# Performance work log

Hardware: AMD Instinct MI355X
Metric: run time of the kernel (lower is better)

## Reference

```python
import jax, jax.numpy as jnp
import numpy as np

B, S, D = 4, 2048, 1024
E, H, TOP_K = 8, 4096, 2


def setup_inputs() -> dict:
    key = jax.random.key(0)
    ks = jax.random.split(key, 5)
    scale = 0.02
    return {
        "x": jax.random.normal(ks[0], (B, S, D), dtype=jnp.float32),
        "Wr": jax.random.normal(ks[1], (D, E), dtype=jnp.float32) * scale,
        "br": jnp.zeros((E,), dtype=jnp.float32),
        "W1": jax.random.normal(ks[2], (E, D, H), dtype=jnp.float32) * scale,
        "b1": jnp.zeros((E, H), dtype=jnp.float32),
        "W2": jax.random.normal(ks[3], (E, H, D), dtype=jnp.float32) * scale,
        "b2": jnp.zeros((E, D), dtype=jnp.float32),
    }


def reference(x, Wr, br, W1, b1, W2, b2):
    b, s, d = x.shape
    xf = x.reshape(-1, d)                                   # [T, D]
    gate = jax.nn.softmax(xf @ Wr + br, axis=-1)            # [T, E]
    top_w, top_i = jax.lax.top_k(gate, TOP_K)               # [T, K]
    top_w = top_w / jnp.sum(top_w, axis=-1, keepdims=True)
    # combine[t, e] = sum_i top_w[t, i] * 1{top_i[t, i] == e}
    combine = jnp.sum(jax.nn.one_hot(top_i, E, dtype=xf.dtype) * top_w[..., None], axis=1)  # [T, E]
    # Dense all-expert FFN (same math as the masked per-expert loops in torch)
    h = jax.nn.gelu(jnp.einsum('td,edh->teh', xf, W1) + b1, approximate=False)  # [T, E, H]
    out = jnp.einsum('teh,ehd,te->td', h, W2, combine) + combine @ b2           # [T, D]
    return out.reshape(b, s, d)
```

## Files before the change

kernel.cpp:

```cpp
#include <hip/hip_runtime.h>
#include <cstdio>


#define T_TOK 8192
#define DIM   1024
#define NEXP  8
#define HID   4096
#define MAXR  18432

typedef float          f32x4   __attribute__((ext_vector_type(4)));
typedef short          bf16x8  __attribute__((ext_vector_type(8)));
typedef unsigned short u16x8   __attribute__((ext_vector_type(8)));
typedef unsigned short u16x4   __attribute__((ext_vector_type(4)));

static __device__ __forceinline__ unsigned short f2bf(float f) {
  unsigned int u = __builtin_bit_cast(unsigned int, f);
  u = (u + 0x7FFFu + ((u >> 16) & 1u)) >> 16;
  return (unsigned short)u;
}

static __device__ __forceinline__ void gl16(const void* g, void* l) {
  __builtin_amdgcn_global_load_lds(
      (const __attribute__((address_space(1))) unsigned int*)g,
      (__attribute__((address_space(3))) unsigned int*)l,
      16, 0, 0);
}

static __device__ __forceinline__ void transpose_body(const float* __restrict__ W,
                                                      unsigned short* __restrict__ WT,
                                                      int R, int C, int bx, int by, int e,
                                                      unsigned int* tl) {
  int t = threadIdx.x;
  int r0 = by * 128, c0 = bx * 128;
  const float* src = W + (size_t)e * R * C + (size_t)r0 * C + c0;
  int cg = t & 31, ph = t >> 5;
  int c4 = cg * 4;
#pragma unroll
  for (int u = 0; u < 8; ++u) {
    int p = u * 8 + ph;
    float4 f0 = *(const float4*)(src + (size_t)(2 * p) * C + c4);
    float4 f1 = *(const float4*)(src + (size_t)(2 * p + 1) * C + c4);
    unsigned int v0 = ((unsigned)f2bf(f1.x) << 16) | f2bf(f0.x);
    unsigned int v1 = ((unsigned)f2bf(f1.y) << 16) | f2bf(f0.y);
    unsigned int v2 = ((unsigned)f2bf(f1.z) << 16) | f2bf(f0.z);
    unsigned int v3 = ((unsigned)f2bf(f1.w) << 16) | f2bf(f0.w);
    *(uint4*)(tl + p * 132 + c4) = make_uint4(v0, v1, v2, v3);
  }
  __syncthreads();
  int rg = t & 15, ch = t >> 4;
  unsigned short* dst = WT + (size_t)e * R * C + (size_t)c0 * R + r0 + rg * 8;
#pragma unroll
  for (int u = 0; u < 8; ++u) {
    int c = ch + u * 16;
    u16x8 o;
#pragma unroll
    for (int j = 0; j < 4; ++j) {
      unsigned int v = tl[(rg * 4 + j) * 132 + c];
      o[2 * j]     = (unsigned short)(v & 0xffff);
      o[2 * j + 1] = (unsigned short)(v >> 16);
    }
    *(u16x8*)(dst + (size_t)c * R) = o;
  }
}

static __device__ __forceinline__ void router_body(int blk, const float* __restrict__ x,
                                                   const float* __restrict__ Wr,
                                                   const float* __restrict__ br,
                                                   int* __restrict__ meta,
                                                   int2* __restrict__ top_i,
                                                   float2* __restrict__ top_w) {
  int lane = threadIdx.x & 63;
  int wid  = threadIdx.x >> 6;
  int t = blk * 4 + wid;
  const float* xp = x + (size_t)t * DIM + lane * 16;
  float acc[NEXP];
#pragma unroll
  for (int e = 0; e < NEXP; ++e) acc[e] = 0.f;
#pragma unroll
  for (int j = 0; j < 16; j += 4) {
    float4 xv = *(const float4*)(xp + j);
    const float* wp = Wr + (size_t)(lane * 16 + j) * NEXP;
#pragma unroll
    for (int jj = 0; jj < 4; ++jj) {
      float xs = jj == 0 ? xv.x : jj == 1 ? xv.y : jj == 2 ? xv.z : xv.w;
      float4 w0 = *(const float4*)(wp + jj * NEXP);
      float4 w1 = *(const float4*)(wp + jj * NEXP + 4);
      acc[0] += xs * w0.x; acc[1] += xs * w0.y; acc[2] += xs * w0.z; acc[3] += xs * w0.w;
      acc[4] += xs * w1.x; acc[5] += xs * w1.y; acc[6] += xs * w1.z; acc[7] += xs * w1.w;
    }
  }
#pragma unroll
  for (int off = 32; off > 0; off >>= 1) {
#pragma unroll
    for (int e = 0; e < NEXP; ++e) acc[e] += __shfl_xor(acc[e], off);
  }
  if (lane == 0) {
    float l[NEXP];
#pragma unroll
    for (int e = 0; e < NEXP; ++e) l[e] = acc[e] + br[e];
    int e1 = 0;
#pragma unroll
    for (int e = 1; e < NEXP; ++e) if (l[e] > l[e1]) e1 = e;
    int e2 = (e1 == 0) ? 1 : 0;
#pragma unroll
    for (int e = 0; e < NEXP; ++e) if (e != e1 && l[e] > l[e2]) e2 = e;
    float g  = expf(l[e2] - l[e1]);
    float w1 = 1.f / (1.f + g);
    top_i[t] = make_int2(e1, e2);
    top_w[t] = make_float2(w1, 1.f - w1);
    atomicAdd(&meta[e1], 1);
    atomicAdd(&meta[e2], 1);
  }
}

__global__ __launch_bounds__(256) void prep_k(const float* __restrict__ W1,
                                              const float* __restrict__ W2,
                                              unsigned short* __restrict__ W1bT,
                                              unsigned short* __restrict__ W2bT,
                                              const float* __restrict__ x,
                                              const float* __restrict__ Wr,
                                              const float* __restrict__ br,
                                              int* __restrict__ meta,
                                              int2* __restrict__ top_i,
                                              float2* __restrict__ top_w,
                                              int* __restrict__ tok_of_row,
                                              float* __restrict__ wt_of_row,
                                              unsigned short* __restrict__ xb) {
  __shared__ __align__(16) unsigned int tl[64 * 132];
  int id = blockIdx.x;
  if (id < 2048) {
    int rem = id & 255;
    transpose_body(W1, W1bT, DIM, HID, rem & 31, rem >> 5, id >> 8, tl);
  } else if (id < 4096) {
    int id2 = id - 2048;
    int rem = id2 & 255;
    transpose_body(W2, W2bT, HID, DIM, rem & 7, rem >> 3, id2 >> 8, tl);
  } else if (id < 6144) {
    router_body(id - 4096, x, Wr, br, meta, top_i, top_w);
  } else if (id < 6216) {
    int i = (id - 6144) * 256 + threadIdx.x;
    if (i < MAXR) { tok_of_row[i] = 0; wt_of_row[i] = 0.f; }
  } else {
    size_t o = (size_t)(id - 6216) * 4096 + (size_t)threadIdx.x * 16;
#pragma unroll
    for (int h = 0; h < 2; ++h) {
      float4 a = *(const float4*)(x + o + h * 8);
      float4 b = *(const float4*)(x + o + h * 8 + 4);
      u16x8 v;
      v[0] = f2bf(a.x); v[1] = f2bf(a.y); v[2] = f2bf(a.z); v[3] = f2bf(a.w);
      v[4] = f2bf(b.x); v[5] = f2bf(b.y); v[6] = f2bf(b.z); v[7] = f2bf(b.w);
      *(u16x8*)(xb + o + h * 8) = v;
    }
  }
}

__global__ void prefix_k(int* __restrict__ meta) {
  if (threadIdx.x == 0) {
    int s = 0;
#pragma unroll
    for (int e = 0; e < NEXP; ++e) {
      meta[16 + e] = s;
      s += (meta[e] + 255) & ~255;
    }
    meta[24] = s;
    meta[25] = s;
  }
}

__global__ __launch_bounds__(256) void scatter_k(const int2* __restrict__ top_i,
                                                 const float2* __restrict__ top_w,
                                                 int* __restrict__ meta,
                                                 int* __restrict__ row_of,
                                                 int* __restrict__ tok_of_row,
                                                 float* __restrict__ wt_of_row) {
  int t = blockIdx.x * 256 + threadIdx.x;
  int2  ei = top_i[t];
  float2 w = top_w[t];
  int p = atomicAdd(&meta[8 + ei.x], 1);
  int r = meta[16 + ei.x] + p;
  tok_of_row[r] = t; wt_of_row[r] = w.x; row_of[t * 2] = r;
  p = atomicAdd(&meta[8 + ei.y], 1);
  r = meta[16 + ei.y] + p;
  tok_of_row[r] = t; wt_of_row[r] = w.y; row_of[t * 2 + 1] = r;
}


template <int KTOT, int NTOT, int EPI, bool INDIR>
__global__ __launch_bounds__(256, 4) void gemmv16_k(const unsigned short* __restrict__ A,
                                                    const unsigned short* __restrict__ Bt,
                                                    const float* __restrict__ bias,
                                                    const int* __restrict__ meta,
                                                    const float* __restrict__ wt_of_row,
                                                    const int* __restrict__ tok_of_row,
                                                    void* __restrict__ Cout) {
  constexpr int NN  = NTOT / 128;
  constexpr int NXB = MAXR / 128;
  constexpr int NWG = NXB * NN;
  constexpr int NSR = NXB / 4;
  constexpr int NKT = KTOT / 64;
  __shared__ __align__(16) unsigned short lds[16384];

  int id = ((int)blockIdx.x & 7) * (NWG / 8) + ((int)blockIdx.x >> 3);
  int sid = id >> 4, sub = id & 15;
  int row0 = ((sid % NSR) * 4 + (sub & 3)) * 128;
  int n0   = ((sid / NSR) * 4 + (sub >> 2)) * 128;
  if (row0 >= meta[25]) return;
  int e = 0;
  while (meta[17 + e] <= row0) ++e;
  if (row0 - meta[16 + e] >= meta[e]) return;
  const unsigned short* Bp = Bt + (size_t)e * NTOT * KTOT;

  int tid = threadIdx.x;
  int lane = tid & 63, wid = tid >> 6;
  int wm = wid >> 1, wn = wid & 1;

  int s = (tid & 7) ^ ((tid >> 3) & 7);
  const unsigned short* pA[4];
#pragma unroll
  for (int i = 0; i < 4; ++i) {
    int r = row0 + (tid >> 3) + i * 32;
    if constexpr (INDIR) {
      pA[i] = A + (size_t)tok_of_row[r] * KTOT + s * 8;
    } else {
      pA[i] = A + (size_t)r * KTOT + s * 8;
    }
  }
  const unsigned short* pB = Bp + (size_t)(n0 + (tid >> 3)) * KTOT + s * 8;

  int am = lane & 15, g = lane >> 4;
  int sw0 = ((0 * 4 + g) ^ (am & 7)) * 8;
  int sw1 = ((1 * 4 + g) ^ (am & 7)) * 8;
  int aRow = (wm * 64 + am) * 64;
  int bRow = 8192 + (wn * 64 + am) * 64;

  f32x4 acc[4][4];
#pragma unroll
  for (int i = 0; i < 4; ++i)
#pragma unroll
    for (int j = 0; j < 4; ++j) acc[i][j] = (f32x4){0.f, 0.f, 0.f, 0.f};

  for (int kt = 0; kt < NKT; ++kt) {
    __syncthreads();
#pragma unroll
    for (int i = 0; i < 4; ++i) {
      gl16(pA[i] + kt * 64, lds + i * 2048 + tid * 8);
      gl16(pB + (size_t)(i * 32) * KTOT + kt * 64, lds + 8192 + i * 2048 + tid * 8);
    }
    __syncthreads();
#pragma unroll
    for (int kk = 0; kk < 2; ++kk) {
      int sw = kk ? sw1 : sw0;
      bf16x8 af[4], bv[4];
#pragma unroll
      for (int i = 0; i < 4; ++i)
        af[i] = *(const bf16x8*)(lds + aRow + i * 1024 + sw);
#pragma unroll
      for (int j = 0; j < 4; ++j)
        bv[j] = *(const bf16x8*)(lds + bRow + j * 1024 + sw);
#pragma unroll
      for (int i = 0; i < 4; ++i)
#pragma unroll
        for (int j = 0; j < 4; ++j)
          acc[i][j] = __builtin_amdgcn_mfma_f32_16x16x32_bf16(af[i], bv[j], acc[i][j], 0, 0, 0);
    }
  }

  int rbase = row0 + wm * 64 + (g << 2);
  int nbase = n0 + wn * 64 + am;
  if constexpr (EPI == 0) {
    unsigned short* Hp = (unsigned short*)Cout;
    const float* bp = bias + (size_t)e * NTOT;
#pragma unroll
    for (int i = 0; i < 4; ++i)
#pragma unroll
      for (int j = 0; j < 4; ++j) {
        int n = nbase + j * 16;
        float bv = bp[n];
#pragma unroll
        for (int gg = 0; gg < 4; ++gg) {
          int m = rbase + i * 16 + gg;
          float v = acc[i][j][gg] + bv;
          v = 0.5f * v * (1.f + erff(v * 0.70710678118654752f));
          Hp[(size_t)m * NTOT + n] = f2bf(v);
        }
      }
  } else {
    float* Op = (float*)Cout;
    const float* bp = bias + (size_t)e * NTOT;
#pragma unroll
    for (int i = 0; i < 4; ++i)
#pragma unroll
      for (int gg = 0; gg < 4; ++gg) {
        int m = rbase + i * 16 + gg;
        float wt = wt_of_row[m];
        if (wt != 0.f) {
          float* orow = Op + (size_t)tok_of_row[m] * DIM;
#pragma unroll
          for (int j = 0; j < 4; ++j) {
            int n = nbase + j * 16;
            atomicAdd(orow + n, (acc[i][j][gg] + bp[n]) * wt);
          }
        }
      }
  }
}

extern "C" void kernel_launch(void* const* d_in, const int* in_sizes, int n_in,
                              void* d_out, int out_size, void* d_ws, size_t ws_size,
                              hipStream_t stream) {
  const float* x  = (const float*)d_in[0];
  const float* Wr = (const float*)d_in[1];
  const float* br = (const float*)d_in[2];
  const float* W1 = (const float*)d_in[3];
  const float* b1 = (const float*)d_in[4];
  const float* W2 = (const float*)d_in[5];
  const float* b2 = (const float*)d_in[6];
  float* out = (float*)d_out;

  char* base = (char*)d_ws;
  size_t off = 0;
  auto carve = [&](size_t bytes) -> void* {
    void* r = base + off;
    off = (off + bytes + 255) & ~(size_t)255;
    return r;
  };
  int*            meta       = (int*)carve(26 * 4);
  int2*           top_i      = (int2*)carve((size_t)T_TOK * 8);
  float2*         top_w      = (float2*)carve((size_t)T_TOK * 8);
  int*            row_of     = (int*)carve((size_t)T_TOK * 2 * 4);
  int*            tok_of_row = (int*)carve((size_t)MAXR * 4);
  float*          wt_of_row  = (float*)carve((size_t)MAXR * 4);
  unsigned short* xb         = (unsigned short*)carve((size_t)T_TOK * DIM * 2);
  unsigned short* W1bT       = (unsigned short*)carve((size_t)NEXP * DIM * HID * 2);
  unsigned short* W2bT       = (unsigned short*)carve((size_t)NEXP * DIM * HID * 2);
  unsigned short* hbuf       = (unsigned short*)carve((size_t)MAXR * HID * 2);
  if (off > ws_size) {
    fprintf(stderr, "kernel_launch: ws_size too small: need %zu have %zu\n", off, ws_size);
    return;
  }

  hipMemsetAsync(meta, 0, 26 * 4, stream);
  hipMemsetAsync(out, 0, (size_t)out_size * 4, stream);
  hipLaunchKernelGGL(prep_k, dim3(8264), dim3(256), 0, stream,
                     W1, W2, W1bT, W2bT, x, Wr, br, meta, top_i, top_w,
                     tok_of_row, wt_of_row, xb);
  hipLaunchKernelGGL(prefix_k, dim3(1), dim3(64), 0, stream, meta);
  hipLaunchKernelGGL(scatter_k, dim3(T_TOK / 256), dim3(256), 0, stream,
                     top_i, top_w, meta, row_of, tok_of_row, wt_of_row);
  hipLaunchKernelGGL((gemmv16_k<DIM, HID, 0, true>), dim3((MAXR / 128) * (HID / 128)),
                     dim3(256), 0, stream,
                     xb, W1bT, b1, meta, wt_of_row, tok_of_row, (void*)hbuf);
  hipLaunchKernelGGL((gemmv16_k<HID, DIM, 1, false>), dim3((MAXR / 128) * (DIM / 128)),
                     dim3(256), 0, stream,
                     hbuf, W2bT, b2, meta, wt_of_row, tok_of_row, (void*)out);
}
```

Measured before the change: 801.8 us.

## Fuse fp32-to-bf16 weight conversion into GEMM B-tile loading, drop pre-transpose pass

Removes the separate transpose and bf16 conversion of W1/W2 from the prep kernel. Each GEMM workgroup now loads fp32 weight tiles directly, converts them to bf16 in registers and writes them into a swizzled LDS layout. This avoids writing and re-reading 128 MB of transposed bf16 weights. In exchange, every M-tile re-reads fp32 weights, which doubles the B bytes per tile and adds conversion ALU work inside the GEMM loop. Synchronous register loads also replace the async global_load_lds path, and the occupancy hint of 4 waves per SIMD is dropped.

Measured after the change: 1.092 ms. 1.36x slower.

```diff
diff --git a/kernel.cpp b/kernel.cpp
--- a/kernel.cpp
+++ b/kernel.cpp
@@ -24,43 +24,6 @@
       (const __attribute__((address_space(1))) unsigned int*)g,
       (__attribute__((address_space(3))) unsigned int*)l,
       16, 0, 0);
-}
-
-static __device__ __forceinline__ void transpose_body(const float* __restrict__ W,
-                                                      unsigned short* __restrict__ WT,
-                                                      int R, int C, int bx, int by, int e,
-                                                      unsigned int* tl) {
-  int t = threadIdx.x;
-  int r0 = by * 128, c0 = bx * 128;
-  const float* src = W + (size_t)e * R * C + (size_t)r0 * C + c0;
-  int cg = t & 31, ph = t >> 5;
-  int c4 = cg * 4;
-#pragma unroll
-  for (int u = 0; u < 8; ++u) {
-    int p = u * 8 + ph;
-    float4 f0 = *(const float4*)(src + (size_t)(2 * p) * C + c4);
-    float4 f1 = *(const float4*)(src + (size_t)(2 * p + 1) * C + c4);
-    unsigned int v0 = ((unsigned)f2bf(f1.x) << 16) | f2bf(f0.x);
-    unsigned int v1 = ((unsigned)f2bf(f1.y) << 16) | f2bf(f0.y);
-    unsigned int v2 = ((unsigned)f2bf(f1.z) << 16) | f2bf(f0.z);
-    unsigned int v3 = ((unsigned)f2bf(f1.w) << 16) | f2bf(f0.w);
-    *(uint4*)(tl + p * 132 + c4) = make_uint4(v0, v1, v2, v3);
-  }
-  __syncthreads();
-  int rg = t & 15, ch = t >> 4;
-  unsigned short* dst = WT + (size_t)e * R * C + (size_t)c0 * R + r0 + rg * 8;
-#pragma unroll
-  for (int u = 0; u < 8; ++u) {
-    int c = ch + u * 16;
-    u16x8 o;
-#pragma unroll
-    for (int j = 0; j < 4; ++j) {
-      unsigned int v = tl[(rg * 4 + j) * 132 + c];
-      o[2 * j]     = (unsigned short)(v & 0xffff);
-      o[2 * j + 1] = (unsigned short)(v >> 16);
-    }
-    *(u16x8*)(dst + (size_t)c * R) = o;
-  }
 }
 
 static __device__ __forceinline__ void router_body(int blk, const float* __restrict__ x,
@@ -113,11 +76,7 @@
   }
 }
 
-__global__ __launch_bounds__(256) void prep_k(const float* __restrict__ W1,
-                                              const float* __restrict__ W2,
-                                              unsigned short* __restrict__ W1bT,
-                                              unsigned short* __restrict__ W2bT,
-                                              const float* __restrict__ x,
+__global__ __launch_bounds__(256) void prep_k(const float* __restrict__ x,
                                               const float* __restrict__ Wr,
                                               const float* __restrict__ br,
                                               int* __restrict__ meta,
@@ -126,22 +85,14 @@
                                               int* __restrict__ tok_of_row,
                                               float* __restrict__ wt_of_row,
                                               unsigned short* __restrict__ xb) {
-  __shared__ __align__(16) unsigned int tl[64 * 132];
   int id = blockIdx.x;
   if (id < 2048) {
-    int rem = id & 255;
-    transpose_body(W1, W1bT, DIM, HID, rem & 31, rem >> 5, id >> 8, tl);
-  } else if (id < 4096) {
-    int id2 = id - 2048;
-    int rem = id2 & 255;
-    transpose_body(W2, W2bT, HID, DIM, rem & 7, rem >> 3, id2 >> 8, tl);
-  } else if (id < 6144) {
-    router_body(id - 4096, x, Wr, br, meta, top_i, top_w);
-  } else if (id < 6216) {
-    int i = (id - 6144) * 256 + threadIdx.x;
+    router_body(id, x, Wr, br, meta, top_i, top_w);
+  } else if (id < 2120) {
+    int i = (id - 2048) * 256 + threadIdx.x;
     if (i < MAXR) { tok_of_row[i] = 0; wt_of_row[i] = 0.f; }
   } else {
-    size_t o = (size_t)(id - 6216) * 4096 + (size_t)threadIdx.x * 16;
+    size_t o = (size_t)(id - 2120) * 4096 + (size_t)threadIdx.x * 16;
 #pragma unroll
     for (int h = 0; h < 2; ++h) {
       float4 a = *(const float4*)(x + o + h * 8);
@@ -186,13 +137,13 @@
 
 
 template <int KTOT, int NTOT, int EPI, bool INDIR>
-__global__ __launch_bounds__(256, 4) void gemmv16_k(const unsigned short* __restrict__ A,
-                                                    const unsigned short* __restrict__ Bt,
-                                                    const float* __restrict__ bias,
-                                                    const int* __restrict__ meta,
-                                                    const float* __restrict__ wt_of_row,
-                                                    const int* __restrict__ tok_of_row,
-                                                    void* __restrict__ Cout) {
+__global__ __launch_bounds__(256) void gemmv17_k(const unsigned short* __restrict__ A,
+                                                 const float* __restrict__ Wf,
+                                                 const float* __restrict__ bias,
+                                                 const int* __restrict__ meta,
+                                                 const float* __restrict__ wt_of_row,
+                                                 const int* __restrict__ tok_of_row,
+                                                 void* __restrict__ Cout) {
   constexpr int NN  = NTOT / 128;
   constexpr int NXB = MAXR / 128;
   constexpr int NWG = NXB * NN;
@@ -208,7 +159,7 @@
   int e = 0;
   while (meta[17 + e] <= row0) ++e;
   if (row0 - meta[16 + e] >= meta[e]) return;
-  const unsigned short* Bp = Bt + (size_t)e * NTOT * KTOT;
+  const float* We = Wf + (size_t)e * (size_t)KTOT * NTOT;
 
   int tid = threadIdx.x;
   int lane = tid & 63, wid = tid >> 6;
@@ -225,13 +176,20 @@
       pA[i] = A + (size_t)r * KTOT + s * 8;
     }
   }
-  const unsigned short* pB = Bp + (size_t)(n0 + (tid >> 3)) * KTOT + s * 8;
+
+  int n4 = (tid & 31) * 4, bs = tid >> 5;
+  const float* pBf = We + (size_t)(bs * 8) * NTOT + n0 + n4;
+  int bofs[4];
+#pragma unroll
+  for (int i = 0; i < 4; ++i) {
+    int n = n4 + i;
+    bofs[i] = 8192 + n * 64 + ((bs ^ (n & 7) ^ ((n >> 4) & 7)) * 8);
+  }
 
   int am = lane & 15, g = lane >> 4;
-  int sw0 = ((0 * 4 + g) ^ (am & 7)) * 8;
-  int sw1 = ((1 * 4 + g) ^ (am & 7)) * 8;
+  int sa0 = ((0 * 4 + g) ^ (am & 7)) * 8;
+  int sa1 = ((1 * 4 + g) ^ (am & 7)) * 8;
   int aRow = (wm * 64 + am) * 64;
-  int bRow = 8192 + (wn * 64 + am) * 64;
 
   f32x4 acc[4][4];
 #pragma unroll
@@ -242,21 +200,36 @@
   for (int kt = 0; kt < NKT; ++kt) {
     __syncthreads();
 #pragma unroll
-    for (int i = 0; i < 4; ++i) {
+    for (int i = 0; i < 4; ++i)
       gl16(pA[i] + kt * 64, lds + i * 2048 + tid * 8);
-      gl16(pB + (size_t)(i * 32) * KTOT + kt * 64, lds + 8192 + i * 2048 + tid * 8);
+    {
+      const float* src = pBf + (size_t)(kt * 64) * NTOT;
+      float4 f[8];
+#pragma unroll
+      for (int j = 0; j < 8; ++j) f[j] = *(const float4*)(src + (size_t)j * NTOT);
+      u16x8 o[4];
+#pragma unroll
+      for (int j = 0; j < 8; ++j) {
+        o[0][j] = f2bf(f[j].x); o[1][j] = f2bf(f[j].y);
+        o[2][j] = f2bf(f[j].z); o[3][j] = f2bf(f[j].w);
+      }
+#pragma unroll
+      for (int i = 0; i < 4; ++i) *(u16x8*)(lds + bofs[i]) = o[i];
     }
     __syncthreads();
 #pragma unroll
     for (int kk = 0; kk < 2; ++kk) {
-      int sw = kk ? sw1 : sw0;
+      int sa = kk ? sa1 : sa0;
       bf16x8 af[4], bv[4];
 #pragma unroll
       for (int i = 0; i < 4; ++i)
-        af[i] = *(const bf16x8*)(lds + aRow + i * 1024 + sw);
-#pragma unroll
-      for (int j = 0; j < 4; ++j)
-        bv[j] = *(const bf16x8*)(lds + bRow + j * 1024 + sw);
+        af[i] = *(const bf16x8*)(lds + aRow + i * 1024 + sa);
+#pragma unroll
+      for (int j = 0; j < 4; ++j) {
+        int n = wn * 64 + j * 16 + am;
+        int sl = ((kk * 4 + g) ^ (am & 7) ^ ((wn * 4 + j) & 7)) * 8;
+        bv[j] = *(const bf16x8*)(lds + 8192 + n * 64 + sl);
+      }
 #pragma unroll
       for (int i = 0; i < 4; ++i)
 #pragma unroll
@@ -331,8 +304,6 @@
   int*            tok_of_row = (int*)carve((size_t)MAXR * 4);
   float*          wt_of_row  = (float*)carve((size_t)MAXR * 4);
   unsigned short* xb         = (unsigned short*)carve((size_t)T_TOK * DIM * 2);
-  unsigned short* W1bT       = (unsigned short*)carve((size_t)NEXP * DIM * HID * 2);
-  unsigned short* W2bT       = (unsigned short*)carve((size_t)NEXP * DIM * HID * 2);
   unsigned short* hbuf       = (unsigned short*)carve((size_t)MAXR * HID * 2);
   if (off > ws_size) {
     fprintf(stderr, "kernel_launch: ws_size too small: need %zu have %zu\n", off, ws_size);
@@ -341,16 +312,15 @@
 
   hipMemsetAsync(meta, 0, 26 * 4, stream);
   hipMemsetAsync(out, 0, (size_t)out_size * 4, stream);
-  hipLaunchKernelGGL(prep_k, dim3(8264), dim3(256), 0, stream,
-                     W1, W2, W1bT, W2bT, x, Wr, br, meta, top_i, top_w,
-                     tok_of_row, wt_of_row, xb);
+  hipLaunchKernelGGL(prep_k, dim3(4168), dim3(256), 0, stream,
+                     x, Wr, br, meta, top_i, top_w, tok_of_row, wt_of_row, xb);
   hipLaunchKernelGGL(prefix_k, dim3(1), dim3(64), 0, stream, meta);
   hipLaunchKernelGGL(scatter_k, dim3(T_TOK / 256), dim3(256), 0, stream,
                      top_i, top_w, meta, row_of, tok_of_row, wt_of_row);
-  hipLaunchKernelGGL((gemmv16_k<DIM, HID, 0, true>), dim3((MAXR / 128) * (HID / 128)),
+  hipLaunchKernelGGL((gemmv17_k<DIM, HID, 0, true>), dim3((MAXR / 128) * (HID / 128)),
                      dim3(256), 0, stream,
-                     xb, W1bT, b1, meta, wt_of_row, tok_of_row, (void*)hbuf);
-  hipLaunchKernelGGL((gemmv16_k<HID, DIM, 1, false>), dim3((MAXR / 128) * (DIM / 128)),
+                     xb, W1, b1, meta, wt_of_row, tok_of_row, (void*)hbuf);
+  hipLaunchKernelGGL((gemmv17_k<HID, DIM, 1, false>), dim3((MAXR / 128) * (DIM / 128)),
                      dim3(256), 0, stream,
-                     hbuf, W2bT, b2, meta, wt_of_row, tok_of_row, (void*)out);
-}
+                     hbuf, W2, b2, meta, wt_of_row, tok_of_row, (void*)out);
+}
```

## Overlap W2 transpose with first expert GEMM in one interleaved launch

Applied to the files above, without the earlier changes.

Moves the W2 fp32-to-bf16 transpose out of the prep kernel and into the first GEMM kernel. There, every third block in the first 6144 transposes a W2 tile while the rest run GEMM1 tiles. The memory-bound transpose can then overlap with the compute-bound GEMM1 and shorten the prep stage. In exchange, the fused kernel uses the larger shared buffer and the GEMM's launch bounds for transpose blocks, and the block interleaving could change the GEMM tile ordering and cache locality.

Result: no change. 787.5 us (-1.8%).

```diff
diff --git a/kernel.cpp b/kernel.cpp
--- a/kernel.cpp
+++ b/kernel.cpp
@@ -113,35 +113,29 @@
   }
 }
 
-__global__ __launch_bounds__(256) void prep_k(const float* __restrict__ W1,
-                                              const float* __restrict__ W2,
-                                              unsigned short* __restrict__ W1bT,
-                                              unsigned short* __restrict__ W2bT,
-                                              const float* __restrict__ x,
-                                              const float* __restrict__ Wr,
-                                              const float* __restrict__ br,
-                                              int* __restrict__ meta,
-                                              int2* __restrict__ top_i,
-                                              float2* __restrict__ top_w,
-                                              int* __restrict__ tok_of_row,
-                                              float* __restrict__ wt_of_row,
-                                              unsigned short* __restrict__ xb) {
+__global__ __launch_bounds__(256) void prep1_k(const float* __restrict__ W1,
+                                               unsigned short* __restrict__ W1bT,
+                                               const float* __restrict__ x,
+                                               const float* __restrict__ Wr,
+                                               const float* __restrict__ br,
+                                               int* __restrict__ meta,
+                                               int2* __restrict__ top_i,
+                                               float2* __restrict__ top_w,
+                                               int* __restrict__ tok_of_row,
+                                               float* __restrict__ wt_of_row,
+                                               unsigned short* __restrict__ xb) {
   __shared__ __align__(16) unsigned int tl[64 * 132];
   int id = blockIdx.x;
   if (id < 2048) {
     int rem = id & 255;
     transpose_body(W1, W1bT, DIM, HID, rem & 31, rem >> 5, id >> 8, tl);
   } else if (id < 4096) {
-    int id2 = id - 2048;
-    int rem = id2 & 255;
-    transpose_body(W2, W2bT, HID, DIM, rem & 7, rem >> 3, id2 >> 8, tl);
-  } else if (id < 6144) {
-    router_body(id - 4096, x, Wr, br, meta, top_i, top_w);
-  } else if (id < 6216) {
-    int i = (id - 6144) * 256 + threadIdx.x;
+    router_body(id - 2048, x, Wr, br, meta, top_i, top_w);
+  } else if (id < 4168) {
+    int i = (id - 4096) * 256 + threadIdx.x;
     if (i < MAXR) { tok_of_row[i] = 0; wt_of_row[i] = 0.f; }
   } else {
-    size_t o = (size_t)(id - 6216) * 4096 + (size_t)threadIdx.x * 16;
+    size_t o = (size_t)(id - 4168) * 4096 + (size_t)threadIdx.x * 16;
 #pragma unroll
     for (int h = 0; h < 2; ++h) {
       float4 a = *(const float4*)(x + o + h * 8);
@@ -186,21 +180,22 @@
 
 
 template <int KTOT, int NTOT, int EPI, bool INDIR>
-__global__ __launch_bounds__(256, 4) void gemmv16_k(const unsigned short* __restrict__ A,
-                                                    const unsigned short* __restrict__ Bt,
-                                                    const float* __restrict__ bias,
-                                                    const int* __restrict__ meta,
-                                                    const float* __restrict__ wt_of_row,
-                                                    const int* __restrict__ tok_of_row,
-                                                    void* __restrict__ Cout) {
+static __device__ __forceinline__ void gemm_body(int rawid,
+                                                 const unsigned short* __restrict__ A,
+                                                 const unsigned short* __restrict__ Bt,
+                                                 const float* __restrict__ bias,
+                                                 const int* __restrict__ meta,
+                                                 const float* __restrict__ wt_of_row,
+                                                 const int* __restrict__ tok_of_row,
+                                                 void* __restrict__ Cout,
+                                                 unsigned short* lds) {
   constexpr int NN  = NTOT / 128;
   constexpr int NXB = MAXR / 128;
   constexpr int NWG = NXB * NN;
   constexpr int NSR = NXB / 4;
   constexpr int NKT = KTOT / 64;
-  __shared__ __align__(16) unsigned short lds[16384];
-
-  int id = ((int)blockIdx.x & 7) * (NWG / 8) + ((int)blockIdx.x >> 3);
+
+  int id = (rawid & 7) * (NWG / 8) + (rawid >> 3);
   int sid = id >> 4, sub = id & 15;
   int row0 = ((sid % NSR) * 4 + (sub & 3)) * 128;
   int n0   = ((sid / NSR) * 4 + (sub >> 2)) * 128;
@@ -303,6 +298,42 @@
         }
       }
   }
+}
+
+__global__ __launch_bounds__(256, 4) void g1w2_k(const unsigned short* __restrict__ xb,
+                                                 const unsigned short* __restrict__ W1bT,
+                                                 const float* __restrict__ W2,
+                                                 unsigned short* __restrict__ W2bT,
+                                                 const float* __restrict__ b1,
+                                                 const int* __restrict__ meta,
+                                                 const float* __restrict__ wt_of_row,
+                                                 const int* __restrict__ tok_of_row,
+                                                 unsigned short* __restrict__ hbuf) {
+  __shared__ __align__(16) unsigned char smem[64 * 132 * 4];
+  int p = blockIdx.x;
+  if (p < 6144 && (p % 3) == 2) {
+    int id2 = p / 3;
+    int rem = id2 & 255;
+    transpose_body(W2, W2bT, HID, DIM, rem & 7, rem >> 3, id2 >> 8,
+                   (unsigned int*)smem);
+  } else {
+    int rawid = (p < 6144) ? (p - p / 3) : (p - 2048);
+    gemm_body<DIM, HID, 0, true>(rawid, xb, W1bT, b1, meta, wt_of_row,
+                                 tok_of_row, (void*)hbuf,
+                                 (unsigned short*)smem);
+  }
+}
+
+__global__ __launch_bounds__(256, 4) void gemm2_k(const unsigned short* __restrict__ hbuf,
+                                                  const unsigned short* __restrict__ W2bT,
+                                                  const float* __restrict__ b2,
+                                                  const int* __restrict__ meta,
+                                                  const float* __restrict__ wt_of_row,
+                                                  const int* __restrict__ tok_of_row,
+                                                  float* __restrict__ out) {
+  __shared__ __align__(16) unsigned short lds[16384];
+  gemm_body<HID, DIM, 1, false>((int)blockIdx.x, hbuf, W2bT, b2, meta,
+                                wt_of_row, tok_of_row, (void*)out, lds);
 }
 
 extern "C" void kernel_launch(void* const* d_in, const int* in_sizes, int n_in,
@@ -341,16 +372,14 @@
 
   hipMemsetAsync(meta, 0, 26 * 4, stream);
   hipMemsetAsync(out, 0, (size_t)out_size * 4, stream);
-  hipLaunchKernelGGL(prep_k, dim3(8264), dim3(256), 0, stream,
-                     W1, W2, W1bT, W2bT, x, Wr, br, meta, top_i, top_w,
+  hipLaunchKernelGGL(prep1_k, dim3(6216), dim3(256), 0, stream,
+                     W1, W1bT, x, Wr, br, meta, top_i, top_w,
                      tok_of_row, wt_of_row, xb);
   hipLaunchKernelGGL(prefix_k, dim3(1), dim3(64), 0, stream, meta);
   hipLaunchKernelGGL(scatter_k, dim3(T_TOK / 256), dim3(256), 0, stream,
                      top_i, top_w, meta, row_of, tok_of_row, wt_of_row);
-  hipLaunchKernelGGL((gemmv16_k<DIM, HID, 0, true>), dim3((MAXR / 128) * (HID / 128)),
-                     dim3(256), 0, stream,
-                     xb, W1bT, b1, meta, wt_of_row, tok_of_row, (void*)hbuf);
-  hipLaunchKernelGGL((gemmv16_k<HID, DIM, 1, false>), dim3((MAXR / 128) * (DIM / 128)),
-                     dim3(256), 0, stream,
-                     hbuf, W2bT, b2, meta, wt_of_row, tok_of_row, (void*)out);
-}
+  hipLaunchKernelGGL(g1w2_k, dim3(6656), dim3(256), 0, stream,
+                     xb, W1bT, W2, W2bT, b1, meta, wt_of_row, tok_of_row, hbuf);
+  hipLaunchKernelGGL(gemm2_k, dim3((MAXR / 128) * (DIM / 128)), dim3(256), 0, stream,
+                     hbuf, W2bT, b2, meta, wt_of_row, tok_of_row, out);
+}
```
